# Kernel optimization log

Measured on AMD Instinct MI355X. Metric: run time of the kernel, lower is better.

## Reference

```python
import jax, jax.numpy as jnp
import numpy as np

B, L, H, NH, NB = 4, 200, 256, 4, 2
HS = H // NH
NEG = -(2.0 ** 32) + 1.0  # torch uses (-2**32 + 1) as mask fill
EPS = 1e-8


def _ln(x, g, b):
    m = x.mean(-1, keepdims=True)
    v = ((x - m) ** 2).mean(-1, keepdims=True)
    return (x - m) / jnp.sqrt(v + EPS) * g + b


def _split_heads(x):  # [B,L,H] -> (NH,B,L,HS), matches torch split(dim=2)+cat(dim=0)
    return x.reshape(x.shape[0], x.shape[1], NH, HS).transpose(2, 0, 1, 3)


def _split_heads4(x):  # [B,L,L,H] -> (NH,B,L,L,HS)
    return x.reshape(B, L, L, NH, HS).transpose(3, 0, 1, 2, 4)


def setup_inputs() -> dict:
    key = jax.random.key(0)
    ks = jax.random.split(key, 20)
    w = 0.05
    inp = {
        "log_seqs": jax.random.randint(ks[0], (B, L), 0, 50000),
        "time_matrices": jax.random.randint(ks[1], (B, L, L), 0, 257),
        "dis_matrices": jax.random.randint(ks[2], (B, L, L), 0, 257),
        "item_embs": jax.random.normal(ks[3], (50001, H), jnp.float32) * w,
        "pos_K_tab": jax.random.normal(ks[4], (L, H), jnp.float32) * w,
        "pos_V_tab": jax.random.normal(ks[5], (L, H), jnp.float32) * w,
        "time_K_tab": jax.random.normal(ks[6], (257, H), jnp.float32) * w,
        "time_V_tab": jax.random.normal(ks[7], (257, H), jnp.float32) * w,
        "dis_K_tab": jax.random.normal(ks[8], (257, H), jnp.float32) * w,
        "dis_V_tab": jax.random.normal(ks[9], (257, H), jnp.float32) * w,
        "ln1_g": jnp.ones((NB, H), jnp.float32),
        "ln1_b": jnp.zeros((NB, H), jnp.float32),
        "Wq": jax.random.normal(ks[10], (NB, H, H), jnp.float32) * w,
        "bq": jnp.zeros((NB, H), jnp.float32),
        "Wk": jax.random.normal(ks[11], (NB, H, H), jnp.float32) * w,
        "bk": jnp.zeros((NB, H), jnp.float32),
        "Wv": jax.random.normal(ks[12], (NB, H, H), jnp.float32) * w,
        "bv": jnp.zeros((NB, H), jnp.float32),
        "ln2_g": jnp.ones((NB, H), jnp.float32),
        "ln2_b": jnp.zeros((NB, H), jnp.float32),
        "W1": jax.random.normal(ks[13], (NB, H, H), jnp.float32) * w,
        "b1": jnp.zeros((NB, H), jnp.float32),
        "W2": jax.random.normal(ks[14], (NB, H, H), jnp.float32) * w,
        "b2": jnp.zeros((NB, H), jnp.float32),
        "lnf_g": jnp.ones((H,), jnp.float32),
        "lnf_b": jnp.zeros((H,), jnp.float32),
    }
    return inp


def _seq2feats(log_seqs, time_matrices, dis_matrices, item_embs,
               pos_K_tab, pos_V_tab, time_K_tab, time_V_tab, dis_K_tab, dis_V_tab,
               ln1_g, ln1_b, Wq, bq, Wk, bk, Wv, bv,
               ln2_g, ln2_b, W1, b1, W2, b2, lnf_g, lnf_b):
    # embedded relative matrices: (NH,B,L,L,HS)
    tK = _split_heads4(time_K_tab[time_matrices])
    tV = _split_heads4(time_V_tab[time_matrices])
    dK = _split_heads4(dis_K_tab[dis_matrices])
    dV = _split_heads4(dis_V_tab[dis_matrices])
    pK = pos_K_tab.reshape(L, NH, HS).transpose(1, 0, 2)  # (NH,L,HS), same for every batch row
    pV = pos_V_tab.reshape(L, NH, HS).transpose(1, 0, 2)

    pad = (log_seqs == 0)  # [B,L]
    keep = (~pad)[..., None].astype(jnp.float32)
    seqs = item_embs[log_seqs] * keep

    causal = ~jnp.tril(jnp.ones((L, L), dtype=bool))  # strictly upper
    mask = pad[None, :, :, None] | causal[None, None, :, :]  # (1,B,L,L) broadcast over heads
    scale = jnp.sqrt(jnp.float32(HS))

    for i in range(NB):
        Qn = _ln(seqs, ln1_g[i], ln1_b[i])
        Qh = _split_heads(Qn @ Wq[i].T + bq[i])
        Kh = _split_heads(seqs @ Wk[i].T + bk[i])
        Vh = _split_heads(seqs @ Wv[i].T + bv[i])
        s = (jnp.einsum('hbqd,hbkd->hbqk', Qh, Kh)
             + jnp.einsum('hbqd,hkd->hbqk', Qh, pK)
             + jnp.einsum('hbqkd,hbqd->hbqk', tK, Qh)
             + jnp.einsum('hbqkd,hbqd->hbqk', dK, Qh)) / scale
        s = jnp.where(mask, NEG, s)
        A = jax.nn.softmax(s, axis=-1)  # (NH,B,L,L)
        o = (jnp.einsum('hbqk,hbkd->hbqd', A, Vh)
             + jnp.einsum('hbqk,hkd->hbqd', A, pV)
             + jnp.einsum('hbqk,hbqkd->hbqd', A, tV)
             + jnp.einsum('hbqk,hbqkd->hbqd', A, dV))
        mha = o.transpose(1, 2, 0, 3).reshape(B, L, H)
        seqs = Qn + mha
        x = _ln(seqs, ln2_g[i], ln2_b[i])
        h = jax.nn.relu(x @ W1[i].T + b1[i])  # Conv1d k=1 == pointwise linear
        seqs = (h @ W2[i].T + b2[i]) + x
        seqs = seqs * keep
    return _ln(seqs, lnf_g, lnf_b)


def reference(log_seqs, time_matrices, dis_matrices, item_embs,
              pos_K_tab, pos_V_tab, time_K_tab, time_V_tab, dis_K_tab, dis_V_tab,
              ln1_g, ln1_b, Wq, bq, Wk, bk, Wv, bv,
              ln2_g, ln2_b, W1, b1, W2, b2, lnf_g, lnf_b):
    return _seq2feats(log_seqs, time_matrices, dis_matrices, item_embs,
                      pos_K_tab, pos_V_tab, time_K_tab, time_V_tab, dis_K_tab, dis_V_tab,
                      ln1_g, ln1_b, Wq, bq, Wk, bk, Wv, bv,
                      ln2_g, ln2_b, W1, b1, W2, b2, lnf_g, lnf_b)
```

## Files before the change

kernel.cpp:

```cpp
#include <hip/hip_runtime.h>
#include <math.h>

typedef __fp16 h2 __attribute__((ext_vector_type(2)));
typedef __fp16 f16x8 __attribute__((ext_vector_type(8)));
typedef float f32x4 __attribute__((ext_vector_type(4)));

#define Bc 4
#define Lc 200
#define Hc 256
#define NHc 4
#define HSc 64
#define NBc 2
#define Mtot (Bc*Lc)
#define TROW 34
#define LDH 264
#define WN (2*Hc*Hc)
#define TN (257*Hc)

static __device__ __forceinline__ float neg_fill() { return -4294967295.0f; }
static __device__ __forceinline__ int rl(int x) { return __builtin_amdgcn_readfirstlane(x); }

static __device__ __forceinline__ uint pkh2(float a, float b) {
  h2 r = __builtin_amdgcn_cvt_pkrtz(a, b);
  return __builtin_bit_cast(uint, r);
}
static __device__ __forceinline__ h2 u2h(uint u) { return __builtin_bit_cast(h2, u); }
#if __has_builtin(__builtin_amdgcn_fdot2)
static __device__ __forceinline__ float dot2(uint a, uint b, float c) {
  return __builtin_amdgcn_fdot2(u2h(a), u2h(b), c, false);
}
#else
static __device__ __forceinline__ float dot2(uint a, uint b, float c) {
  h2 x = u2h(a), y = u2h(b);
  return c + (float)x.x * (float)y.x + (float)x.y * (float)y.y;
}
#endif
static __device__ __forceinline__ float h2f(ushort u) {
  return (float)__builtin_bit_cast(_Float16, u);
}

__global__ void cvtw_k(const float* __restrict__ Wq, const float* __restrict__ Wk,
                       const float* __restrict__ Wv, const float* __restrict__ W1,
                       const float* __restrict__ W2,
                       const float* __restrict__ tK, const float* __restrict__ tV,
                       const float* __restrict__ dK, const float* __restrict__ dV,
                       ushort* __restrict__ out) {
  int y = blockIdx.y;
  const float* src;
  int n, off;
  if (y < 5) {
    n = WN; off = y * WN;
    src = (y == 0) ? Wq : (y == 1) ? Wk : (y == 2) ? Wv : (y == 3) ? W1 : W2;
  } else {
    n = TN; off = 5 * WN + (y - 5) * TN;
    src = (y == 5) ? tK : (y == 6) ? tV : (y == 7) ? dK : dV;
  }
  int idx = (blockIdx.x * 256 + threadIdx.x) * 8;
  if (idx >= n) return;
  float4 a = *(const float4*)&src[idx];
  float4 b = *(const float4*)&src[idx + 4];
  uint4 o;
  o.x = pkh2(a.x, a.y); o.y = pkh2(a.z, a.w);
  o.z = pkh2(b.x, b.y); o.w = pkh2(b.z, b.w);
  *(uint4*)&out[off + idx] = o;
}

__global__ __launch_bounds__(256)
void mmqkv_k(const float* __restrict__ seqs, const float* __restrict__ emb,
             const int* __restrict__ logs, int useEmb,
             const float* __restrict__ g, const float* __restrict__ bt,
             const ushort* __restrict__ Wq16, const ushort* __restrict__ Wk16,
             const ushort* __restrict__ Wv16,
             const float* __restrict__ bq, const float* __restrict__ bk,
             const float* __restrict__ bv,
             const float* __restrict__ pK, const float* __restrict__ pV,
             float* __restrict__ Qn,
             ushort* __restrict__ Q16, ushort* __restrict__ K16,
             ushort* __restrict__ V16) {
  __shared__ __fp16 Al[16][LDH];
  __shared__ __fp16 Wl[64][LDH];
  int m0 = blockIdx.x * 16;
  int y = blockIdx.y;
  int region = y >> 2, nloc = (y & 3) * 64;
  const ushort* Wsrc = (region == 0) ? Wq16 : (region == 1 ? Wk16 : Wv16);
  const float* bias = (region == 0) ? bq : (region == 1 ? bk : bv);
  int t = threadIdx.x;
  if (region == 0) {
    int r = t >> 4, c0 = (t & 15) * 16;
    int m = m0 + r;
    const float* xr;
    bool zero = false;
    if (useEmb) {
      int tok = logs[m];
      zero = (tok == 0);
      xr = &emb[tok * Hc + c0];
    } else {
      xr = &seqs[m * Hc + c0];
    }
    float4 v0, v1, v2, v3;
    if (zero) {
      v0 = v1 = v2 = v3 = make_float4(0.f, 0.f, 0.f, 0.f);
    } else {
      v0 = *(const float4*)&xr[0];
      v1 = *(const float4*)&xr[4];
      v2 = *(const float4*)&xr[8];
      v3 = *(const float4*)&xr[12];
    }
    float s = v0.x + v0.y + v0.z + v0.w + v1.x + v1.y + v1.z + v1.w
            + v2.x + v2.y + v2.z + v2.w + v3.x + v3.y + v3.z + v3.w;
    float q = v0.x*v0.x + v0.y*v0.y + v0.z*v0.z + v0.w*v0.w
            + v1.x*v1.x + v1.y*v1.y + v1.z*v1.z + v1.w*v1.w
            + v2.x*v2.x + v2.y*v2.y + v2.z*v2.z + v2.w*v2.w
            + v3.x*v3.x + v3.y*v3.y + v3.z*v3.z + v3.w*v3.w;
#pragma unroll
    for (int o = 1; o < 16; o <<= 1) { s += __shfl_xor(s, o); q += __shfl_xor(q, o); }
    float mean = s * (1.f / Hc);
    float var = q * (1.f / Hc) - mean * mean;
    float rstd = 1.f / sqrtf(var + 1e-8f);
    float tmp[16] = {v0.x,v0.y,v0.z,v0.w,v1.x,v1.y,v1.z,v1.w,
                     v2.x,v2.y,v2.z,v2.w,v3.x,v3.y,v3.z,v3.w};
    float nv[16];
#pragma unroll
    for (int j = 0; j < 16; ++j)
      nv[j] = (tmp[j] - mean) * rstd * g[c0 + j] + bt[c0 + j];
#pragma unroll
    for (int j = 0; j < 16; j += 2)
      *(h2*)&Al[r][c0 + j] = __builtin_amdgcn_cvt_pkrtz(nv[j], nv[j + 1]);
    if (y == 0) {
#pragma unroll
      for (int j = 0; j < 16; j += 4)
        *(float4*)&Qn[m * Hc + c0 + j] = make_float4(nv[j], nv[j+1], nv[j+2], nv[j+3]);
    }
  } else {
    for (int i = t; i < 16 * 64; i += 256) {
      int r = i >> 6, c = (i & 63) * 4;
      int m = m0 + r;
      float4 v;
      if (useEmb) {
        int tok = logs[m];
        v = (tok == 0) ? make_float4(0.f, 0.f, 0.f, 0.f)
                       : *(const float4*)&emb[tok * Hc + c];
      } else {
        v = *(const float4*)&seqs[m * Hc + c];
      }
      *(h2*)&Al[r][c] = __builtin_amdgcn_cvt_pkrtz(v.x, v.y);
      *(h2*)&Al[r][c + 2] = __builtin_amdgcn_cvt_pkrtz(v.z, v.w);
    }
  }
  for (int i = t; i < 2048; i += 256) {
    int r = i >> 5, c = (i & 31) * 8;
    uint4 v = *(const uint4*)&Wsrc[(nloc + r) * Hc + c];
    *(uint4*)&Wl[r][c] = v;
  }
  __syncthreads();
  int wave = t >> 6, lane = t & 63;
  int row = lane & 15, kg = lane >> 4;
  int bn = wave * 16 + row;
  f32x4 acc = {0.f, 0.f, 0.f, 0.f};
#pragma unroll
  for (int k0 = 0; k0 < Hc; k0 += 32) {
    int kk = k0 + kg * 8;
    f16x8 a = *(const f16x8*)&Al[row][kk];
    f16x8 bb = *(const f16x8*)&Wl[bn][kk];
    acc = __builtin_amdgcn_mfma_f32_16x16x32_f16(a, bb, acc, 0, 0, 0);
  }
  int coln = nloc + wave * 16 + row;
  ushort* op = (region == 0) ? Q16 : (region == 1 ? K16 : V16);
  const float* pT = (region == 1) ? pK : pV;
#pragma unroll
  for (int r = 0; r < 4; ++r) {
    int m = m0 + kg * 4 + r;
    float v = acc[r] + bias[coln];
    if (region) v += pT[(m % Lc) * Hc + coln];
    op[m * Hc + coln] = __builtin_bit_cast(ushort, (_Float16)v);
  }
}

__global__ __launch_bounds__(1024, 4)
void attn_k(const uint* __restrict__ Q16, const uint* __restrict__ K16,
            const ushort* __restrict__ V16,
            const ushort* __restrict__ tK16, const ushort* __restrict__ dK16,
            const ushort* __restrict__ tV16, const ushort* __restrict__ dV16,
            const int* __restrict__ tm, const int* __restrict__ dm,
            const int* __restrict__ logs,
            const float* __restrict__ Qn, float* __restrict__ seqs) {
  int h = blockIdx.x, b = blockIdx.y, bz = blockIdx.z;
  __shared__ uint tKs[257 * TROW];
  __shared__ uint dKs[257 * TROW];
  __shared__ uint tVs[257 * TROW];
  __shared__ uint dVs[257 * TROW];
  __shared__ float sArow[16][204];
  int t = threadIdx.x;
  {
    const ushort* tabs[4] = {tK16, dK16, tV16, dV16};
    uint* dsts[4] = {tKs, dKs, tVs, dVs};
#pragma unroll
    for (int tb = 0; tb < 4; ++tb) {
      const ushort* s = tabs[tb] + h * HSc;
      uint* d = dsts[tb];
      for (int i = t; i < 257 * 8; i += 1024) {
        int r = i >> 3, c = (i & 7) * 8;
        uint4 v = *(const uint4*)&s[r * Hc + c];
        *(uint4*)&d[r * TROW + (c >> 1)] = v;
      }
    }
  }
  __syncthreads();
  int wave = t >> 6, lane = t & 63;
  int z = h * 4 + b;
  int q = wave * 16 + bz;
  if (q >= Lc) return;
  int m = b * Lc + q;
  int oi = m * Hc + h * HSc + lane;
  if (logs[m] == 0) { seqs[oi] = Qn[oi]; return; }
  const int* tmr = tm + rl(m * Lc);
  const int* dmr = dm + rl(m * Lc);
  const uint* Qr = Q16 + rl(m * (Hc / 2) + h * (HSc / 2));
  uint qreg[32];
#pragma unroll
  for (int u = 0; u < 32; ++u) qreg[u] = Qr[u];
  int np = (q >> 6) + 1;
  float sv[4];
  float mx = neg_fill();
#pragma unroll
  for (int p = 0; p < 4; ++p) {
    sv[p] = neg_fill();
    if (p >= np) continue;
    int k = p * 64 + lane;
    int kc = (k <= q) ? k : q;
    int ti = tmr[kc], di = dmr[kc];
    const uint2* tr = (const uint2*)&tKs[ti * TROW];
    const uint2* dr = (const uint2*)&dKs[di * TROW];
    const uint4* Kr = (const uint4*)&K16[(b * Lc + kc) * (Hc / 2) + h * (HSc / 2)];
    float a0 = 0.f, a1 = 0.f;
#pragma unroll
    for (int u = 0; u < 8; ++u) {
      uint4 kv = Kr[u];
      uint2 tv0 = tr[2 * u], tv1 = tr[2 * u + 1];
      uint2 dv0 = dr[2 * u], dv1 = dr[2 * u + 1];
      a0 = dot2(qreg[4 * u + 0], kv.x, a0);  a1 = dot2(qreg[4 * u + 1], kv.y, a1);
      a0 = dot2(qreg[4 * u + 2], kv.z, a0);  a1 = dot2(qreg[4 * u + 3], kv.w, a1);
      a0 = dot2(qreg[4 * u + 0], tv0.x, a0); a1 = dot2(qreg[4 * u + 1], tv0.y, a1);
      a0 = dot2(qreg[4 * u + 2], tv1.x, a0); a1 = dot2(qreg[4 * u + 3], tv1.y, a1);
      a0 = dot2(qreg[4 * u + 0], dv0.x, a0); a1 = dot2(qreg[4 * u + 1], dv0.y, a1);
      a0 = dot2(qreg[4 * u + 2], dv1.x, a0); a1 = dot2(qreg[4 * u + 3], dv1.y, a1);
    }
    if (k <= q) sv[p] = (a0 + a1) * 0.125f;
    mx = fmaxf(mx, sv[p]);
  }
#pragma unroll
  for (int o = 32; o; o >>= 1) mx = fmaxf(mx, __shfl_xor(mx, o));
  float sum = 0.f;
  float ev[4];
#pragma unroll
  for (int p = 0; p < 4; ++p) {
    ev[p] = __expf(sv[p] - mx);
    sum += ev[p];
  }
#pragma unroll
  for (int o = 32; o; o >>= 1) sum += __shfl_xor(sum, o);
  float rs = 1.f / sum;
#pragma unroll
  for (int p = 0; p < 4; ++p) {
    if (p >= np) continue;
    int k = p * 64 + lane;
    if (k < Lc) sArow[wave][k] = ev[p] * rs;
  }
  for (int k = q + 1 + lane; k < 204; k += 64) sArow[wave][k] = 0.f;
  int half = lane >> 5, li = lane & 31;
  const uint* Vu = (const uint*)V16 + rl(b * Lc * (Hc / 2) + h * (HSc / 2)) + li;
  float acc0 = 0.f, acc1 = 0.f, acc2 = 0.f, acc3 = 0.f;
  for (int k0 = 0; k0 <= q; k0 += 4) {
    int ka = k0 + half;
    int kb = k0 + 2 + half;
    int kca = (ka <= q) ? ka : q;
    int kcb = (kb <= q) ? kb : q;
    float aa = sArow[wave][ka];
    float ab = sArow[wave][kb];
    int ti0 = tmr[kca], di0 = dmr[kca];
    int ti1 = tmr[kcb], di1 = dmr[kcb];
    uint tv0 = tVs[ti0 * TROW + li];
    uint dv0 = dVs[di0 * TROW + li];
    uint vv0 = Vu[kca * (Hc / 2)];
    uint tv1 = tVs[ti1 * TROW + li];
    uint dv1 = dVs[di1 * TROW + li];
    uint vv1 = Vu[kcb * (Hc / 2)];
    h2 s0 = u2h(tv0) + u2h(dv0) + u2h(vv0);
    h2 s1 = u2h(tv1) + u2h(dv1) + u2h(vv1);
    acc0 = fmaf(aa, (float)s0.x, acc0);
    acc1 = fmaf(aa, (float)s0.y, acc1);
    acc2 = fmaf(ab, (float)s1.x, acc2);
    acc3 = fmaf(ab, (float)s1.y, acc3);
  }
  float accLo = acc0 + acc2; accLo += __shfl_xor(accLo, 32);
  float accHi = acc1 + acc3; accHi += __shfl_xor(accHi, 32);
  if (half == 0) {
    int oib = m * Hc + h * HSc + 2 * li;
    float2 qv = *(const float2*)&Qn[oib];
    float2 r;
    r.x = qv.x + accLo;
    r.y = qv.y + accHi;
    *(float2*)&seqs[oib] = r;
  }
}

template <int FIN>
__global__ __launch_bounds__(512)
void ffn_k(float* __restrict__ seqs,
           const float* __restrict__ g, const float* __restrict__ bt,
           const ushort* __restrict__ W1_16, const float* __restrict__ b1,
           const ushort* __restrict__ W2_16, const float* __restrict__ b2,
           const int* __restrict__ logs,
           const float* __restrict__ lnf_g, const float* __restrict__ lnf_b,
           float* __restrict__ dout) {
  __shared__ __fp16 Xl[16][LDH];
  __shared__ __fp16 Hl[16][LDH];
  __shared__ __fp16 Wl[128][LDH];
  __shared__ float Ol[16][Hc];
  int m0 = blockIdx.x * 16;
  int t = threadIdx.x;
  {
    int r = t >> 5, c0 = (t & 31) * 8;
    const float* xr = &seqs[(m0 + r) * Hc + c0];
    float4 v0 = *(const float4*)&xr[0];
    float4 v1 = *(const float4*)&xr[4];
    float s = v0.x + v0.y + v0.z + v0.w + v1.x + v1.y + v1.z + v1.w;
    float q = v0.x*v0.x + v0.y*v0.y + v0.z*v0.z + v0.w*v0.w
            + v1.x*v1.x + v1.y*v1.y + v1.z*v1.z + v1.w*v1.w;
#pragma unroll
    for (int o = 1; o < 32; o <<= 1) { s += __shfl_xor(s, o); q += __shfl_xor(q, o); }
    float mean = s * (1.f / Hc);
    float var = q * (1.f / Hc) - mean * mean;
    float rstd = 1.f / sqrtf(var + 1e-8f);
    float tmp[8] = {v0.x,v0.y,v0.z,v0.w,v1.x,v1.y,v1.z,v1.w};
    float nv[8];
#pragma unroll
    for (int j = 0; j < 8; ++j)
      nv[j] = (tmp[j] - mean) * rstd * g[c0 + j] + bt[c0 + j];
#pragma unroll
    for (int j = 0; j < 8; j += 2)
      *(h2*)&Xl[r][c0 + j] = __builtin_amdgcn_cvt_pkrtz(nv[j], nv[j + 1]);
  }
  int wave = t >> 6, lane = t & 63;
  int row = lane & 15, kg = lane >> 4;
#pragma unroll
  for (int ch = 0; ch < 2; ++ch) {
    __syncthreads();
    for (int i = t; i < 4096; i += 512) {
      int r = i >> 5, c = (i & 31) * 8;
      uint4 v = *(const uint4*)&W1_16[(ch * 128 + r) * Hc + c];
      *(uint4*)&Wl[r][c] = v;
    }
    __syncthreads();
    int bn = wave * 16 + row;
    f32x4 acc = {0.f, 0.f, 0.f, 0.f};
#pragma unroll
    for (int k0 = 0; k0 < Hc; k0 += 32) {
      int kk = k0 + kg * 8;
      f16x8 a = *(const f16x8*)&Xl[row][kk];
      f16x8 bb = *(const f16x8*)&Wl[bn][kk];
      acc = __builtin_amdgcn_mfma_f32_16x16x32_f16(a, bb, acc, 0, 0, 0);
    }
    int coln = ch * 128 + wave * 16 + row;
    float bv = b1[coln];
#pragma unroll
    for (int r = 0; r < 4; ++r) {
      float v = fmaxf(acc[r] + bv, 0.f);
      Hl[kg * 4 + r][coln] = (_Float16)v;
    }
  }
#pragma unroll
  for (int ch = 0; ch < 2; ++ch) {
    __syncthreads();
    for (int i = t; i < 4096; i += 512) {
      int r = i >> 5, c = (i & 31) * 8;
      uint4 v = *(const uint4*)&W2_16[(ch * 128 + r) * Hc + c];
      *(uint4*)&Wl[r][c] = v;
    }
    __syncthreads();
    int bn = wave * 16 + row;
    f32x4 acc = {0.f, 0.f, 0.f, 0.f};
#pragma unroll
    for (int k0 = 0; k0 < Hc; k0 += 32) {
      int kk = k0 + kg * 8;
      f16x8 a = *(const f16x8*)&Hl[row][kk];
      f16x8 bb = *(const f16x8*)&Wl[bn][kk];
      acc = __builtin_amdgcn_mfma_f32_16x16x32_f16(a, bb, acc, 0, 0, 0);
    }
    int coln = ch * 128 + wave * 16 + row;
    float bv = b2[coln];
#pragma unroll
    for (int r = 0; r < 4; ++r) {
      int mrow = kg * 4 + r;
      int m = m0 + mrow;
      float keep = (logs[m] != 0) ? 1.f : 0.f;
      float xv = h2f(__builtin_bit_cast(ushort, Xl[mrow][coln]));
      float val = (acc[r] + bv + xv) * keep;
      if (FIN) Ol[mrow][coln] = val;
      else     seqs[m * Hc + coln] = val;
    }
  }
  if (FIN) {
    __syncthreads();
    int r = t >> 5, c0 = (t & 31) * 8;
    float v[8];
#pragma unroll
    for (int j = 0; j < 8; ++j) v[j] = Ol[r][c0 + j];
    float s = 0.f, q = 0.f;
#pragma unroll
    for (int j = 0; j < 8; ++j) { s += v[j]; q += v[j] * v[j]; }
#pragma unroll
    for (int o = 1; o < 32; o <<= 1) { s += __shfl_xor(s, o); q += __shfl_xor(q, o); }
    float mean = s * (1.f / Hc);
    float var = q * (1.f / Hc) - mean * mean;
    float rstd = 1.f / sqrtf(var + 1e-8f);
#pragma unroll
    for (int j = 0; j < 8; ++j)
      dout[(m0 + r) * Hc + c0 + j] = (v[j] - mean) * rstd * lnf_g[c0 + j] + lnf_b[c0 + j];
  }
}

extern "C" void kernel_launch(void* const* d_in, const int* in_sizes, int n_in,
                              void* d_out, int out_size, void* d_ws, size_t ws_size,
                              hipStream_t stream) {
  const int* logs = (const int*)d_in[0];
  const int* tm   = (const int*)d_in[1];
  const int* dm   = (const int*)d_in[2];
  const float* item = (const float*)d_in[3];
  const float* pK = (const float*)d_in[4];
  const float* pV = (const float*)d_in[5];
  const float* tK = (const float*)d_in[6];
  const float* tV = (const float*)d_in[7];
  const float* dK = (const float*)d_in[8];
  const float* dV = (const float*)d_in[9];
  const float* ln1_g = (const float*)d_in[10];
  const float* ln1_b = (const float*)d_in[11];
  const float* Wq = (const float*)d_in[12];
  const float* bq = (const float*)d_in[13];
  const float* Wk = (const float*)d_in[14];
  const float* bk = (const float*)d_in[15];
  const float* Wv = (const float*)d_in[16];
  const float* bv = (const float*)d_in[17];
  const float* ln2_g = (const float*)d_in[18];
  const float* ln2_b = (const float*)d_in[19];
  const float* W1 = (const float*)d_in[20];
  const float* b1 = (const float*)d_in[21];
  const float* W2 = (const float*)d_in[22];
  const float* b2 = (const float*)d_in[23];
  const float* lnf_g = (const float*)d_in[24];
  const float* lnf_b = (const float*)d_in[25];

  const int NROW = Mtot * Hc;
  float* ws = (float*)d_ws;
  float* sSeqs = ws + 0 * NROW;
  float* sQn   = ws + 1 * NROW;
  ushort* Q16  = (ushort*)(ws + 2 * NROW);
  ushort* K16  = Q16 + NROW;
  ushort* V16  = K16 + NROW;
  ushort* w16  = (ushort*)(ws + 4 * NROW);
  ushort* wq16 = w16 + 0 * WN;
  ushort* wk16 = w16 + 1 * WN;
  ushort* wv16 = w16 + 2 * WN;
  ushort* w116 = w16 + 3 * WN;
  ushort* w216 = w16 + 4 * WN;
  ushort* tK16 = w16 + 5 * WN;
  ushort* tV16 = tK16 + TN;
  ushort* dK16 = tV16 + TN;
  ushort* dV16 = dK16 + TN;

  dim3 gC(64, 9);
  cvtw_k<<<gC, 256, 0, stream>>>(Wq, Wk, Wv, W1, W2, tK, tV, dK, dV, w16);

  dim3 gQKV(Mtot / 16, 12);
  dim3 ga(NHc, Bc, 16);
  const int HHh = Hc * Hc;
  for (int i = 0; i < NBc; ++i) {
    mmqkv_k<<<gQKV, 256, 0, stream>>>(sSeqs, item, logs, (i == 0) ? 1 : 0,
                                      ln1_g + i * Hc, ln1_b + i * Hc,
                                      wq16 + i * HHh, wk16 + i * HHh, wv16 + i * HHh,
                                      bq + i * Hc, bk + i * Hc, bv + i * Hc,
                                      pK, pV, sQn, Q16, K16, V16);
    attn_k<<<ga, 1024, 0, stream>>>((const uint*)Q16, (const uint*)K16, V16,
                                    tK16, dK16, tV16, dV16,
                                    tm, dm, logs, sQn, sSeqs);
    if (i == 0)
      ffn_k<0><<<Mtot / 16, 512, 0, stream>>>(sSeqs, ln2_g + i * Hc, ln2_b + i * Hc,
                                              w116 + i * HHh, b1 + i * Hc,
                                              w216 + i * HHh, b2 + i * Hc, logs,
                                              nullptr, nullptr, nullptr);
    else
      ffn_k<1><<<Mtot / 16, 512, 0, stream>>>(sSeqs, ln2_g + i * Hc, ln2_b + i * Hc,
                                              w116 + i * HHh, b1 + i * Hc,
                                              w216 + i * HHh, b2 + i * Hc, logs,
                                              lnf_g, lnf_b, (float*)d_out);
  }
}
```

Baseline: 82.82 us.

## Precompute Q·K, Q·timeK, Q·disK tables with MFMA and gather scores

Attention scores are no longer built from per-key dot products against gathered time and distance key rows. Each block now computes its 16 queries against all keys and against all 257 time and distance key table entries with MFMA, stores the results in shared memory, and sums three gathered scalars per score. This swaps O(L·HS) scalar dot2 work per query for a small dense matmul, and drops the tK/dK shared-memory staging. It adds about 47 MFMA tiles per block and roughly 50KB of extra shared memory, which may reduce occupancy.

```diff
diff --git a/kernel.cpp b/kernel.cpp
--- a/kernel.cpp
+++ b/kernel.cpp
@@ -25,16 +25,6 @@
   return __builtin_bit_cast(uint, r);
 }
 static __device__ __forceinline__ h2 u2h(uint u) { return __builtin_bit_cast(h2, u); }
-#if __has_builtin(__builtin_amdgcn_fdot2)
-static __device__ __forceinline__ float dot2(uint a, uint b, float c) {
-  return __builtin_amdgcn_fdot2(u2h(a), u2h(b), c, false);
-}
-#else
-static __device__ __forceinline__ float dot2(uint a, uint b, float c) {
-  h2 x = u2h(a), y = u2h(b);
-  return c + (float)x.x * (float)y.x + (float)x.y * (float)y.y;
-}
-#endif
 static __device__ __forceinline__ float h2f(ushort u) {
   return (float)__builtin_bit_cast(_Float16, u);
 }
@@ -177,7 +167,7 @@
 }
 
 __global__ __launch_bounds__(1024, 4)
-void attn_k(const uint* __restrict__ Q16, const uint* __restrict__ K16,
+void attn_k(const ushort* __restrict__ Q16, const ushort* __restrict__ K16,
             const ushort* __restrict__ V16,
             const ushort* __restrict__ tK16, const ushort* __restrict__ dK16,
             const ushort* __restrict__ tV16, const ushort* __restrict__ dV16,
@@ -185,29 +175,64 @@
             const int* __restrict__ logs,
             const float* __restrict__ Qn, float* __restrict__ seqs) {
   int h = blockIdx.x, b = blockIdx.y, bz = blockIdx.z;
-  __shared__ uint tKs[257 * TROW];
-  __shared__ uint dKs[257 * TROW];
   __shared__ uint tVs[257 * TROW];
   __shared__ uint dVs[257 * TROW];
+  __shared__ float S0l[16][212];
+  __shared__ float Tql[16][272];
+  __shared__ float Dql[16][272];
   __shared__ float sArow[16][204];
   int t = threadIdx.x;
+  int wave = t >> 6, lane = t & 63;
+  int row16 = lane & 15, kg = lane >> 4;
   {
-    const ushort* tabs[4] = {tK16, dK16, tV16, dV16};
-    uint* dsts[4] = {tKs, dKs, tVs, dVs};
-#pragma unroll
-    for (int tb = 0; tb < 4; ++tb) {
-      const ushort* s = tabs[tb] + h * HSc;
-      uint* d = dsts[tb];
-      for (int i = t; i < 257 * 8; i += 1024) {
-        int r = i >> 3, c = (i & 7) * 8;
-        uint4 v = *(const uint4*)&s[r * Hc + c];
-        *(uint4*)&d[r * TROW + (c >> 1)] = v;
+    const ushort* s1 = tV16 + h * HSc;
+    const ushort* s2 = dV16 + h * HSc;
+    for (int i = t; i < 257 * 8; i += 1024) {
+      int r = i >> 3, c = (i & 7) * 8;
+      *(uint4*)&tVs[r * TROW + (c >> 1)] = *(const uint4*)&s1[r * Hc + c];
+      *(uint4*)&dVs[r * TROW + (c >> 1)] = *(const uint4*)&s2[r * Hc + c];
+    }
+  }
+  {
+    int qa = row16 * 16 + bz;
+    bool va = qa < Lc;
+    f16x8 A0 = {0,0,0,0,0,0,0,0}, A1 = A0;
+    if (va) {
+      const ushort* Qr = &Q16[(b * Lc + qa) * Hc + h * HSc];
+      A0 = *(const f16x8*)&Qr[kg * 8];
+      A1 = *(const f16x8*)&Qr[32 + kg * 8];
+    }
+    for (int j = wave; j < 47; j += 16) {
+      int kind, n;
+      if (j < 13) { kind = 0; n = j; }
+      else if (j < 30) { kind = 1; n = j - 13; }
+      else { kind = 2; n = j - 30; }
+      int col = n * 16 + row16;
+      const ushort* Bsrc;
+      bool vb;
+      if (kind == 0) { vb = col < Lc; Bsrc = &K16[(b * Lc + (vb ? col : 0)) * Hc + h * HSc]; }
+      else { vb = col < 257; Bsrc = &((kind == 1) ? tK16 : dK16)[(vb ? col : 0) * Hc + h * HSc]; }
+      f16x8 B0 = {0,0,0,0,0,0,0,0}, B1 = B0;
+      if (vb) {
+        B0 = *(const f16x8*)&Bsrc[kg * 8];
+        B1 = *(const f16x8*)&Bsrc[32 + kg * 8];
       }
+      f32x4 acc = {0.f, 0.f, 0.f, 0.f};
+      acc = __builtin_amdgcn_mfma_f32_16x16x32_f16(A0, B0, acc, 0, 0, 0);
+      acc = __builtin_amdgcn_mfma_f32_16x16x32_f16(A1, B1, acc, 0, 0, 0);
+      if (kind == 0) {
+#pragma unroll
+        for (int r = 0; r < 4; ++r) S0l[kg * 4 + r][col] = acc[r];
+      } else if (kind == 1) {
+#pragma unroll
+        for (int r = 0; r < 4; ++r) Tql[kg * 4 + r][col] = acc[r];
+      } else {
+#pragma unroll
+        for (int r = 0; r < 4; ++r) Dql[kg * 4 + r][col] = acc[r];
+      }
     }
   }
   __syncthreads();
-  int wave = t >> 6, lane = t & 63;
-  int z = h * 4 + b;
   int q = wave * 16 + bz;
   if (q >= Lc) return;
   int m = b * Lc + q;
@@ -215,10 +240,9 @@
   if (logs[m] == 0) { seqs[oi] = Qn[oi]; return; }
   const int* tmr = tm + rl(m * Lc);
   const int* dmr = dm + rl(m * Lc);
-  const uint* Qr = Q16 + rl(m * (Hc / 2) + h * (HSc / 2));
-  uint qreg[32];
-#pragma unroll
-  for (int u = 0; u < 32; ++u) qreg[u] = Qr[u];
+  const float* srow = S0l[wave];
+  const float* trow = Tql[wave];
+  const float* drow = Dql[wave];
   int np = (q >> 6) + 1;
   float sv[4];
   float mx = neg_fill();
@@ -229,23 +253,8 @@
     int k = p * 64 + lane;
     int kc = (k <= q) ? k : q;
     int ti = tmr[kc], di = dmr[kc];
-    const uint2* tr = (const uint2*)&tKs[ti * TROW];
-    const uint2* dr = (const uint2*)&dKs[di * TROW];
-    const uint4* Kr = (const uint4*)&K16[(b * Lc + kc) * (Hc / 2) + h * (HSc / 2)];
-    float a0 = 0.f, a1 = 0.f;
-#pragma unroll
-    for (int u = 0; u < 8; ++u) {
-      uint4 kv = Kr[u];
-      uint2 tv0 = tr[2 * u], tv1 = tr[2 * u + 1];
-      uint2 dv0 = dr[2 * u], dv1 = dr[2 * u + 1];
-      a0 = dot2(qreg[4 * u + 0], kv.x, a0);  a1 = dot2(qreg[4 * u + 1], kv.y, a1);
-      a0 = dot2(qreg[4 * u + 2], kv.z, a0);  a1 = dot2(qreg[4 * u + 3], kv.w, a1);
-      a0 = dot2(qreg[4 * u + 0], tv0.x, a0); a1 = dot2(qreg[4 * u + 1], tv0.y, a1);
-      a0 = dot2(qreg[4 * u + 2], tv1.x, a0); a1 = dot2(qreg[4 * u + 3], tv1.y, a1);
-      a0 = dot2(qreg[4 * u + 0], dv0.x, a0); a1 = dot2(qreg[4 * u + 1], dv0.y, a1);
-      a0 = dot2(qreg[4 * u + 2], dv1.x, a0); a1 = dot2(qreg[4 * u + 3], dv1.y, a1);
-    }
-    if (k <= q) sv[p] = (a0 + a1) * 0.125f;
+    float sc = (srow[kc] + trow[ti] + drow[di]) * 0.125f;
+    if (k <= q) sv[p] = sc;
     mx = fmaxf(mx, sv[p]);
   }
 #pragma unroll
@@ -480,7 +489,7 @@
                                       wq16 + i * HHh, wk16 + i * HHh, wv16 + i * HHh,
                                       bq + i * Hc, bk + i * Hc, bv + i * Hc,
                                       pK, pV, sQn, Q16, K16, V16);
-    attn_k<<<ga, 1024, 0, stream>>>((const uint*)Q16, (const uint*)K16, V16,
+    attn_k<<<ga, 1024, 0, stream>>>(Q16, K16, V16,
                                     tK16, dK16, tV16, dV16,
                                     tm, dm, logs, sQn, sSeqs);
     if (i == 0)
```

New measurement: 75.89 us (median of 3 runs). -8.4%, faster.
